# Kernel tuning notes

Hardware: AMD Instinct MI355X
Metric: run time of the kernel (lower is better)

The kernel has to match this reference:

```python
import jax, jax.numpy as jnp
import numpy as np

B, M, D = 16384, 32, 16
LAYERS = [64, 64, 64]


def setup_inputs() -> dict:
    key = jax.random.key(0)
    ks = jax.random.split(key, 4)
    inp = {"embeddings": jax.random.normal(ks[0], (B, M, D), dtype=jnp.float32)}
    hk_1 = M
    for i, hk in enumerate(LAYERS):
        # glorot-ish scale for W_i of shape (m, Hk_1, Hk)
        scale = (2.0 / (M * hk_1 + hk)) ** 0.5
        inp[f"W{i}"] = jax.random.normal(ks[i + 1], (M, hk_1, hk), dtype=jnp.float32) * scale
        hk_1 = hk
    return inp


def reference(embeddings, W0, W1, W2):
    # embeddings == x0: (B, m, D); W_i: (m, Hk_1, Hk)
    x0 = embeddings
    xk = x0  # x^{k-1}, starts as x0 with Hk_1 = m
    outs = []
    for W in (W0, W1, W2):
        # Fused form of: (x0[:,:,None,:] * xk[:,None,:,:])[..., None] * W -> sum over m, Hk_1
        # then permute to (B, Hk, D) and apply activation.
        xk = jax.nn.relu(jnp.einsum("bmd,bhd,mhk->bkd", x0, xk, W))  # (B, Hk, D)
        outs.append(jnp.sum(xk, axis=2))  # (B, Hk)
    return jnp.concatenate(outs, axis=1)  # (B, sum(layers_dim))
```

## Files before the change

### kernel.cpp

```cpp
#include <hip/hip_runtime.h>


typedef _Float16 half8 __attribute__((ext_vector_type(8)));
typedef float f32x4 __attribute__((ext_vector_type(4)));

#define OUT_STRIDE 192

__global__ void prep_w(const float* __restrict__ W, _Float16* __restrict__ dst,
                       int K, int logH, int nkbLog) {
  int e = blockIdx.x * 256 + threadIdx.x;
  int j = e & 7;
  int lane = (e >> 3) & 63;
  int rr = lane & 15, qq = lane >> 4;
  int rest = e >> 9;
  int nkb = K >> 5;
  int kb = rest & (nkb - 1);
  int t = rest >> nkbLog;
  int k = kb * 32 + qq * 8 + j;
  int H = 1 << logH;
  int m = k >> logH, h = k & (H - 1);
  int n = t * 16 + rr;
  dst[e] = (_Float16)W[(m * H + h) * 64 + n];
}

template<int LOGH, int VROW, int VBSTR, bool LAST>
__device__ __forceinline__ void run_layer(
    const _Float16* __restrict__ Wp, const _Float16* vsrc,
    const _Float16* x0s, _Float16* xkdst, float* __restrict__ out,
    long gb0, int loff, int lane, int r, int q)
{
  const int NKB = 1 << LOGH;
  f32x4 acc[4][4];
#pragma unroll
  for (int b = 0; b < 4; ++b)
#pragma unroll
    for (int t = 0; t < 4; ++t) acc[b][t] = (f32x4){0.f, 0.f, 0.f, 0.f};

#pragma unroll 2
  for (int kb = 0; kb < NKB; ++kb) {
    const int m  = kb >> (LOGH - 5);
    const int h0 = (kb & ((1 << (LOGH - 5)) - 1)) << 5;
    half8 Bf[4];
#pragma unroll
    for (int t = 0; t < 4; ++t)
      Bf[t] = *(const half8*)(Wp + ((size_t)(t * NKB + kb) * 64 + lane) * 8);
#pragma unroll
    for (int b = 0; b < 4; ++b) {
      half8 av = *(const half8*)(vsrc + b * VBSTR + r * VROW + h0 + q * 8);
      _Float16 xs = x0s[b * 640 + r * 40 + m];
      half8 xv;
#pragma unroll
      for (int j = 0; j < 8; ++j) xv[j] = xs;
      half8 af = av * xv;
#pragma unroll
      for (int t = 0; t < 4; ++t)
        acc[b][t] = __builtin_amdgcn_mfma_f32_16x16x32_f16(af, Bf[t], acc[b][t], 0, 0, 0);
    }
  }

#pragma unroll
  for (int b = 0; b < 4; ++b) {
#pragma unroll
    for (int t = 0; t < 4; ++t) {
      float s = 0.f;
#pragma unroll
      for (int rr = 0; rr < 4; ++rr) {
        float v = acc[b][t][rr];
        v = v > 0.f ? v : 0.f;
        s += v;
        if (!LAST)
          xkdst[b * 1152 + (q * 4 + rr) * 72 + t * 16 + r] = (_Float16)v;
      }
      s += __shfl_xor(s, 16);
      s += __shfl_xor(s, 32);
      if (q == 0)
        out[(gb0 + b) * OUT_STRIDE + loff + t * 16 + r] = s;
    }
  }
}

__global__ __launch_bounds__(256, 2) void cin_main(
    const float* __restrict__ emb, const _Float16* __restrict__ Wall,
    float* __restrict__ out)
{
  __shared__ __align__(16) _Float16 lds[28672];
  const int lane = threadIdx.x & 63;
  const int wv = threadIdx.x >> 6;
  const int r = lane & 15, q = lane >> 4;
  const int lb0 = wv * 4;
  const long gb0 = (long)blockIdx.x * 16 + lb0;

  _Float16* x0b = &lds[lb0 * 640];
  _Float16* xkb = &lds[10240 + lb0 * 1152];

#pragma unroll
  for (int bb = 0; bb < 4; ++bb) {
    const float* src = emb + (gb0 + bb) * 512;
    _Float16* dstb = x0b + bb * 640;
#pragma unroll
    for (int i = 0; i < 2; ++i) {
      int f = i * 256 + lane * 4;
      float4 v = *(const float4*)(src + f);
      int m = f >> 4, d = f & 15;
      dstb[(d + 0) * 40 + m] = (_Float16)v.x;
      dstb[(d + 1) * 40 + m] = (_Float16)v.y;
      dstb[(d + 2) * 40 + m] = (_Float16)v.z;
      dstb[(d + 3) * 40 + m] = (_Float16)v.w;
    }
  }

  run_layer<5, 40,  640, false>(Wall,           x0b, x0b, xkb, out, gb0, 0,   lane, r, q);
  run_layer<6, 72, 1152, false>(Wall + 65536,   xkb, x0b, xkb, out, gb0, 64,  lane, r, q);
  run_layer<6, 72, 1152, true >(Wall + 196608,  xkb, x0b, xkb, out, gb0, 128, lane, r, q);
}

extern "C" void kernel_launch(void* const* d_in, const int* in_sizes, int n_in,
                              void* d_out, int out_size, void* d_ws, size_t ws_size,
                              hipStream_t stream) {
  const float* emb = (const float*)d_in[0];
  const float* W0  = (const float*)d_in[1];
  const float* W1  = (const float*)d_in[2];
  const float* W2  = (const float*)d_in[3];
  float* out = (float*)d_out;
  _Float16* ws = (_Float16*)d_ws;

  prep_w<<<256, 256, 0, stream>>>(W0, ws,          1024, 5, 5);
  prep_w<<<512, 256, 0, stream>>>(W1, ws + 65536,  2048, 6, 6);
  prep_w<<<512, 256, 0, stream>>>(W2, ws + 196608, 2048, 6, 6);

  cin_main<<<1024, 256, 0, stream>>>(emb, ws, out);
}
```

Baseline: 215.4 us.

## Switch to 32x32x16 MFMA with software-prefetched operands and fused weight prep

Replaces the 16x16x32 MFMA tiling with 32x32x16 MFMAs, so each wave covers two batch rows per instruction and the weight fragment layout is rebuilt to match. Next-iteration weight, activation and x0 operands are loaded one step ahead to hide load latency. The scale multiply now uses packed half2 operations, and LDS strides are padded to reduce bank conflicts. The three weight-prep launches are merged into one kernel to cut launch overhead, at the cost of more accumulator registers per thread and a more complex epilogue index mapping.

```diff
diff --git a/kernel.cpp b/kernel.cpp
--- a/kernel.cpp
+++ b/kernel.cpp
@@ -2,79 +2,143 @@
 
 
 typedef _Float16 half8 __attribute__((ext_vector_type(8)));
-typedef float f32x4 __attribute__((ext_vector_type(4)));
+typedef _Float16 half2v __attribute__((ext_vector_type(2)));
+typedef float f32x16 __attribute__((ext_vector_type(16)));
 
 #define OUT_STRIDE 192
+#define X0B 648
+#define X0R 40
+#define XKB 1160
+#define XKR 72
 
-__global__ void prep_w(const float* __restrict__ W, _Float16* __restrict__ dst,
-                       int K, int logH, int nkbLog) {
+__global__ void prep_w_all(const float* __restrict__ W0,
+                           const float* __restrict__ W1,
+                           const float* __restrict__ W2,
+                           _Float16* __restrict__ dst) {
   int e = blockIdx.x * 256 + threadIdx.x;
-  int j = e & 7;
-  int lane = (e >> 3) & 63;
-  int rr = lane & 15, qq = lane >> 4;
-  int rest = e >> 9;
-  int nkb = K >> 5;
-  int kb = rest & (nkb - 1);
-  int t = rest >> nkbLog;
-  int k = kb * 32 + qq * 8 + j;
-  int H = 1 << logH;
-  int m = k >> logH, h = k & (H - 1);
-  int n = t * 16 + rr;
+  const float* W;
+  int logH, nkbLog, le;
+  if (e < 65536)       { W = W0; logH = 5; nkbLog = 6; le = e; }
+  else if (e < 196608) { W = W1; logH = 6; nkbLog = 7; le = e - 65536; }
+  else                 { W = W2; logH = 6; nkbLog = 7; le = e - 196608; }
+  int j    = le & 7;
+  int lane = (le >> 3) & 63;
+  int rest = le >> 9;
+  int kb   = rest & ((1 << nkbLog) - 1);
+  int t    = rest >> nkbLog;
+  int k    = kb * 16 + ((lane >> 5) << 3) + j;
+  int H    = 1 << logH;
+  int m    = k >> logH, h = k & (H - 1);
+  int n    = t * 32 + (lane & 31);
   dst[e] = (_Float16)W[(m * H + h) * 64 + n];
 }
 
-template<int LOGH, int VROW, int VBSTR, bool LAST>
+template<int LOGH, int VR, int VB, bool LAST>
 __device__ __forceinline__ void run_layer(
     const _Float16* __restrict__ Wp, const _Float16* vsrc,
     const _Float16* x0s, _Float16* xkdst, float* __restrict__ out,
-    long gb0, int loff, int lane, int r, int q)
+    long gb0, int loff, int lane)
 {
-  const int NKB = 1 << LOGH;
-  f32x4 acc[4][4];
+  const int NIT = 1 << (LOGH + 1);
+  const int HM  = (1 << (LOGH - 4)) - 1;
+  const int SH  = LOGH - 4;
+
+  const int l31 = lane & 31;
+  const int q2  = lane >> 5;
+  const int r16 = lane & 15;
+  const int b4  = (lane >> 4) & 1;
+
+  const _Float16* avb[2];
+  const _Float16* xsb[2];
 #pragma unroll
-  for (int b = 0; b < 4; ++b)
+  for (int bp = 0; bp < 2; ++bp) {
+    int bl = bp * 2 + b4;
+    avb[bp] = vsrc + bl * VB + r16 * VR + q2 * 8;
+    xsb[bp] = x0s + bl * X0B + r16 * X0R;
+  }
+  const _Float16* Wl = Wp + lane * 8;
+
+  f32x16 acc[2][2];
 #pragma unroll
-    for (int t = 0; t < 4; ++t) acc[b][t] = (f32x4){0.f, 0.f, 0.f, 0.f};
+  for (int bp = 0; bp < 2; ++bp)
+#pragma unroll
+    for (int t = 0; t < 2; ++t)
+#pragma unroll
+      for (int g = 0; g < 16; ++g) acc[bp][t][g] = 0.f;
 
-#pragma unroll 2
-  for (int kb = 0; kb < NKB; ++kb) {
-    const int m  = kb >> (LOGH - 5);
-    const int h0 = (kb & ((1 << (LOGH - 5)) - 1)) << 5;
-    half8 Bf[4];
+  half8  Bc[2], avc[2];
+  half2v xc[2];
 #pragma unroll
-    for (int t = 0; t < 4; ++t)
-      Bf[t] = *(const half8*)(Wp + ((size_t)(t * NKB + kb) * 64 + lane) * 8);
+  for (int t = 0; t < 2; ++t)
+    Bc[t] = *(const half8*)(Wl + (size_t)(t * NIT) * 512);
 #pragma unroll
-    for (int b = 0; b < 4; ++b) {
-      half8 av = *(const half8*)(vsrc + b * VBSTR + r * VROW + h0 + q * 8);
-      _Float16 xs = x0s[b * 640 + r * 40 + m];
-      half8 xv;
+  for (int bp = 0; bp < 2; ++bp) {
+    avc[bp] = *(const half8*)(avb[bp]);
+    _Float16 x = xsb[bp][0];
+    xc[bp] = (half2v){x, x};
+  }
+
+#pragma unroll 4
+  for (int kb = 0; kb < NIT; ++kb) {
+    half8  Bn[2], avn[2];
+    half2v xn[2];
+    const bool more = (kb + 1) < NIT;
+    if (more) {
+      const int kn = kb + 1;
 #pragma unroll
-      for (int j = 0; j < 8; ++j) xv[j] = xs;
-      half8 af = av * xv;
+      for (int t = 0; t < 2; ++t)
+        Bn[t] = *(const half8*)(Wl + (size_t)(t * NIT + kn) * 512);
+      const int hb = (kn & HM) * 16;
+      const int mn = kn >> SH;
 #pragma unroll
-      for (int t = 0; t < 4; ++t)
-        acc[b][t] = __builtin_amdgcn_mfma_f32_16x16x32_f16(af, Bf[t], acc[b][t], 0, 0, 0);
+      for (int bp = 0; bp < 2; ++bp) {
+        avn[bp] = *(const half8*)(avb[bp] + hb);
+        _Float16 x = xsb[bp][mn];
+        xn[bp] = (half2v){x, x};
+      }
+    }
+    half8 af[2];
+#pragma unroll
+    for (int bp = 0; bp < 2; ++bp) {
+      half2v* ap = (half2v*)&af[bp];
+      half2v* vp = (half2v*)&avc[bp];
+#pragma unroll
+      for (int j2 = 0; j2 < 4; ++j2) ap[j2] = vp[j2] * xc[bp];
+    }
+#pragma unroll
+    for (int bp = 0; bp < 2; ++bp)
+#pragma unroll
+      for (int t = 0; t < 2; ++t)
+        acc[bp][t] = __builtin_amdgcn_mfma_f32_32x32x16_f16(
+            af[bp], Bc[t], acc[bp][t], 0, 0, 0);
+    if (more) {
+#pragma unroll
+      for (int t = 0; t < 2; ++t) Bc[t] = Bn[t];
+#pragma unroll
+      for (int bp = 0; bp < 2; ++bp) { avc[bp] = avn[bp]; xc[bp] = xn[bp]; }
     }
   }
 
 #pragma unroll
-  for (int b = 0; b < 4; ++b) {
+  for (int bp = 0; bp < 2; ++bp) {
 #pragma unroll
-    for (int t = 0; t < 4; ++t) {
-      float s = 0.f;
+    for (int t = 0; t < 2; ++t) {
+      float s[2] = {0.f, 0.f};
 #pragma unroll
-      for (int rr = 0; rr < 4; ++rr) {
-        float v = acc[b][t][rr];
+      for (int g = 0; g < 16; ++g) {
+        float v = acc[bp][t][g];
         v = v > 0.f ? v : 0.f;
-        s += v;
+        const int half = g >> 3;
+        const int g7 = g & 7;
+        const int d = (g7 & 3) + 8 * (g7 >> 2) + 4 * q2;
+        s[half] += v;
         if (!LAST)
-          xkdst[b * 1152 + (q * 4 + rr) * 72 + t * 16 + r] = (_Float16)v;
+          xkdst[(bp * 2 + half) * XKB + d * XKR + t * 32 + l31] = (_Float16)v;
       }
-      s += __shfl_xor(s, 16);
-      s += __shfl_xor(s, 32);
-      if (q == 0)
-        out[(gb0 + b) * OUT_STRIDE + loff + t * 16 + r] = s;
+      s[0] += __shfl_xor(s[0], 32);
+      s[1] += __shfl_xor(s[1], 32);
+      const float sv = q2 ? s[1] : s[0];
+      out[(gb0 + bp * 2 + q2) * OUT_STRIDE + loff + t * 32 + l31] = sv;
     }
   }
 }
@@ -83,35 +147,33 @@
     const float* __restrict__ emb, const _Float16* __restrict__ Wall,
     float* __restrict__ out)
 {
-  __shared__ __align__(16) _Float16 lds[28672];
+  __shared__ __align__(16) _Float16 lds[16 * X0B + 16 * XKB];
   const int lane = threadIdx.x & 63;
   const int wv = threadIdx.x >> 6;
-  const int r = lane & 15, q = lane >> 4;
-  const int lb0 = wv * 4;
-  const long gb0 = (long)blockIdx.x * 16 + lb0;
+  const long gb0 = (long)blockIdx.x * 16 + wv * 4;
 
-  _Float16* x0b = &lds[lb0 * 640];
-  _Float16* xkb = &lds[10240 + lb0 * 1152];
+  _Float16* x0w = &lds[wv * 4 * X0B];
+  _Float16* xkw = &lds[16 * X0B + wv * 4 * XKB];
 
 #pragma unroll
   for (int bb = 0; bb < 4; ++bb) {
     const float* src = emb + (gb0 + bb) * 512;
-    _Float16* dstb = x0b + bb * 640;
+    _Float16* dstb = x0w + bb * X0B;
 #pragma unroll
     for (int i = 0; i < 2; ++i) {
       int f = i * 256 + lane * 4;
       float4 v = *(const float4*)(src + f);
       int m = f >> 4, d = f & 15;
-      dstb[(d + 0) * 40 + m] = (_Float16)v.x;
-      dstb[(d + 1) * 40 + m] = (_Float16)v.y;
-      dstb[(d + 2) * 40 + m] = (_Float16)v.z;
-      dstb[(d + 3) * 40 + m] = (_Float16)v.w;
+      dstb[(d + 0) * X0R + m] = (_Float16)v.x;
+      dstb[(d + 1) * X0R + m] = (_Float16)v.y;
+      dstb[(d + 2) * X0R + m] = (_Float16)v.z;
+      dstb[(d + 3) * X0R + m] = (_Float16)v.w;
     }
   }
 
-  run_layer<5, 40,  640, false>(Wall,           x0b, x0b, xkb, out, gb0, 0,   lane, r, q);
-  run_layer<6, 72, 1152, false>(Wall + 65536,   xkb, x0b, xkb, out, gb0, 64,  lane, r, q);
-  run_layer<6, 72, 1152, true >(Wall + 196608,  xkb, x0b, xkb, out, gb0, 128, lane, r, q);
+  run_layer<5, X0R, X0B, false>(Wall,          x0w, x0w, xkw, out, gb0, 0,   lane);
+  run_layer<6, XKR, XKB, false>(Wall + 65536,  xkw, x0w, xkw, out, gb0, 64,  lane);
+  run_layer<6, XKR, XKB, true >(Wall + 196608, xkw, x0w, xkw, out, gb0, 128, lane);
 }
 
 extern "C" void kernel_launch(void* const* d_in, const int* in_sizes, int n_in,
@@ -124,9 +186,7 @@
   float* out = (float*)d_out;
   _Float16* ws = (_Float16*)d_ws;
 
-  prep_w<<<256, 256, 0, stream>>>(W0, ws,          1024, 5, 5);
-  prep_w<<<512, 256, 0, stream>>>(W1, ws + 65536,  2048, 6, 6);
-  prep_w<<<512, 256, 0, stream>>>(W2, ws + 196608, 2048, 6, 6);
+  prep_w_all<<<1280, 256, 0, stream>>>(W0, W1, W2, ws);
 
   cin_main<<<1024, 256, 0, stream>>>(emb, ws, out);
 }
```

Result: slower. 241.1 us (+11.9%).

## Hoist xk fragments into registers, fuse weight prep launches, raise occupancy

Applied to the files above, without the earlier changes.

The A-operand vectors (x0 and xk rows) are now loaded from LDS into registers once per layer rather than every k-block, and the m loop is restructured so the x0 scalar broadcast is loaded once per m and multiplied with packed half2 ops. The three weight-prep kernels are merged into one launch, and the x0 LDS row stride shrinks from 40 to 32 with launch bounds raised to 3 blocks per CU. The aim is to cut LDS traffic, launch overhead and latency exposure, at the cost of more register pressure and possible LDS bank conflicts from the unpadded stride.

```diff
diff --git a/kernel.cpp b/kernel.cpp
--- a/kernel.cpp
+++ b/kernel.cpp
@@ -2,59 +2,80 @@
 
 
 typedef _Float16 half8 __attribute__((ext_vector_type(8)));
+typedef _Float16 half2v __attribute__((ext_vector_type(2)));
 typedef float f32x4 __attribute__((ext_vector_type(4)));
 
 #define OUT_STRIDE 192
+#define X0R 32
+#define X0B 512
+#define XKR 72
+#define XKB 1152
 
-__global__ void prep_w(const float* __restrict__ W, _Float16* __restrict__ dst,
-                       int K, int logH, int nkbLog) {
+__global__ void prep_w_all(const float* __restrict__ W0,
+                           const float* __restrict__ W1,
+                           const float* __restrict__ W2,
+                           _Float16* __restrict__ dst) {
   int e = blockIdx.x * 256 + threadIdx.x;
-  int j = e & 7;
-  int lane = (e >> 3) & 63;
-  int rr = lane & 15, qq = lane >> 4;
-  int rest = e >> 9;
-  int nkb = K >> 5;
-  int kb = rest & (nkb - 1);
-  int t = rest >> nkbLog;
-  int k = kb * 32 + qq * 8 + j;
-  int H = 1 << logH;
-  int m = k >> logH, h = k & (H - 1);
-  int n = t * 16 + rr;
+  const float* W;
+  int logH, nkbLog, le;
+  if (e < 65536)       { W = W0; logH = 5; nkbLog = 5; le = e; }
+  else if (e < 196608) { W = W1; logH = 6; nkbLog = 6; le = e - 65536; }
+  else                 { W = W2; logH = 6; nkbLog = 6; le = e - 196608; }
+  int j    = le & 7;
+  int lane = (le >> 3) & 63;
+  int rr   = lane & 15, qq = lane >> 4;
+  int rest = le >> 9;
+  int kb   = rest & ((1 << nkbLog) - 1);
+  int t    = rest >> nkbLog;
+  int k    = kb * 32 + qq * 8 + j;
+  int H    = 1 << logH;
+  int m    = k >> logH, h = k & (H - 1);
+  int n    = t * 16 + rr;
   dst[e] = (_Float16)W[(m * H + h) * 64 + n];
 }
 
-template<int LOGH, int VROW, int VBSTR, bool LAST>
+template<int NHI, bool LAST>
 __device__ __forceinline__ void run_layer(
-    const _Float16* __restrict__ Wp, const _Float16* vsrc,
-    const _Float16* x0s, _Float16* xkdst, float* __restrict__ out,
+    const _Float16* __restrict__ Wp, const half8 (&av)[4][NHI],
+    const _Float16* x0s, _Float16* xkw, float* __restrict__ out,
     long gb0, int loff, int lane, int r, int q)
 {
-  const int NKB = 1 << LOGH;
+  const int NKB = 32 * NHI;
   f32x4 acc[4][4];
 #pragma unroll
   for (int b = 0; b < 4; ++b)
 #pragma unroll
     for (int t = 0; t < 4; ++t) acc[b][t] = (f32x4){0.f, 0.f, 0.f, 0.f};
 
+  const _Float16* Wl = Wp + lane * 8;
+
 #pragma unroll 2
-  for (int kb = 0; kb < NKB; ++kb) {
-    const int m  = kb >> (LOGH - 5);
-    const int h0 = (kb & ((1 << (LOGH - 5)) - 1)) << 5;
-    half8 Bf[4];
-#pragma unroll
-    for (int t = 0; t < 4; ++t)
-      Bf[t] = *(const half8*)(Wp + ((size_t)(t * NKB + kb) * 64 + lane) * 8);
+  for (int m = 0; m < 32; ++m) {
+    half2v xs2[4];
 #pragma unroll
     for (int b = 0; b < 4; ++b) {
-      half8 av = *(const half8*)(vsrc + b * VBSTR + r * VROW + h0 + q * 8);
-      _Float16 xs = x0s[b * 640 + r * 40 + m];
-      half8 xv;
+      _Float16 x = x0s[b * X0B + r * X0R + m];
+      xs2[b] = (half2v){x, x};
+    }
 #pragma unroll
-      for (int j = 0; j < 8; ++j) xv[j] = xs;
-      half8 af = av * xv;
+    for (int hi = 0; hi < NHI; ++hi) {
+      const int kb = m * NHI + hi;
+      half8 Bf[4];
 #pragma unroll
       for (int t = 0; t < 4; ++t)
-        acc[b][t] = __builtin_amdgcn_mfma_f32_16x16x32_f16(af, Bf[t], acc[b][t], 0, 0, 0);
+        Bf[t] = *(const half8*)(Wl + (size_t)(t * NKB + kb) * 512);
+#pragma unroll
+      for (int b = 0; b < 4; ++b) {
+        half8 af;
+        half2v* ap = (half2v*)&af;
+        const half2v* vp = (const half2v*)&av[b][hi];
+#pragma unroll
+        for (int j2 = 0; j2 < 4; ++j2) ap[j2] = vp[j2] * xs2[b];
+#pragma unroll
+        for (int t = 0; t < 4; ++t)
+          acc[b][t] = __builtin_amdgcn_mfma_f32_16x16x32_f16(
+              af, Bf[t], acc[b][t], 0, 0, 0);
+      }
     }
   }
 
@@ -69,7 +90,7 @@
         v = v > 0.f ? v : 0.f;
         s += v;
         if (!LAST)
-          xkdst[b * 1152 + (q * 4 + rr) * 72 + t * 16 + r] = (_Float16)v;
+          xkw[b * XKB + (q * 4 + rr) * XKR + t * 16 + r] = (_Float16)v;
       }
       s += __shfl_xor(s, 16);
       s += __shfl_xor(s, 32);
@@ -79,39 +100,55 @@
   }
 }
 
-__global__ __launch_bounds__(256, 2) void cin_main(
+__global__ __launch_bounds__(256, 3) void cin_main(
     const float* __restrict__ emb, const _Float16* __restrict__ Wall,
     float* __restrict__ out)
 {
-  __shared__ __align__(16) _Float16 lds[28672];
+  __shared__ __align__(16) _Float16 lds[16 * X0B + 16 * XKB];
   const int lane = threadIdx.x & 63;
   const int wv = threadIdx.x >> 6;
   const int r = lane & 15, q = lane >> 4;
-  const int lb0 = wv * 4;
-  const long gb0 = (long)blockIdx.x * 16 + lb0;
+  const long gb0 = (long)blockIdx.x * 16 + wv * 4;
 
-  _Float16* x0b = &lds[lb0 * 640];
-  _Float16* xkb = &lds[10240 + lb0 * 1152];
+  _Float16* x0w = &lds[wv * 4 * X0B];
+  _Float16* xkw = &lds[16 * X0B + wv * 4 * XKB];
 
 #pragma unroll
   for (int bb = 0; bb < 4; ++bb) {
     const float* src = emb + (gb0 + bb) * 512;
-    _Float16* dstb = x0b + bb * 640;
+    _Float16* dstb = x0w + bb * X0B;
 #pragma unroll
     for (int i = 0; i < 2; ++i) {
       int f = i * 256 + lane * 4;
       float4 v = *(const float4*)(src + f);
       int m = f >> 4, d = f & 15;
-      dstb[(d + 0) * 40 + m] = (_Float16)v.x;
-      dstb[(d + 1) * 40 + m] = (_Float16)v.y;
-      dstb[(d + 2) * 40 + m] = (_Float16)v.z;
-      dstb[(d + 3) * 40 + m] = (_Float16)v.w;
+      dstb[(d + 0) * X0R + m] = (_Float16)v.x;
+      dstb[(d + 1) * X0R + m] = (_Float16)v.y;
+      dstb[(d + 2) * X0R + m] = (_Float16)v.z;
+      dstb[(d + 3) * X0R + m] = (_Float16)v.w;
     }
   }
 
-  run_layer<5, 40,  640, false>(Wall,           x0b, x0b, xkb, out, gb0, 0,   lane, r, q);
-  run_layer<6, 72, 1152, false>(Wall + 65536,   xkb, x0b, xkb, out, gb0, 64,  lane, r, q);
-  run_layer<6, 72, 1152, true >(Wall + 196608,  xkb, x0b, xkb, out, gb0, 128, lane, r, q);
+  half8 av1[4][1];
+#pragma unroll
+  for (int b = 0; b < 4; ++b)
+    av1[b][0] = *(const half8*)(x0w + b * X0B + r * X0R + q * 8);
+  run_layer<1, false>(Wall, av1, x0w, xkw, out, gb0, 0, lane, r, q);
+
+  half8 av2[4][2];
+#pragma unroll
+  for (int b = 0; b < 4; ++b)
+#pragma unroll
+    for (int hi = 0; hi < 2; ++hi)
+      av2[b][hi] = *(const half8*)(xkw + b * XKB + r * XKR + hi * 32 + q * 8);
+  run_layer<2, false>(Wall + 65536, av2, x0w, xkw, out, gb0, 64, lane, r, q);
+
+#pragma unroll
+  for (int b = 0; b < 4; ++b)
+#pragma unroll
+    for (int hi = 0; hi < 2; ++hi)
+      av2[b][hi] = *(const half8*)(xkw + b * XKB + r * XKR + hi * 32 + q * 8);
+  run_layer<2, true>(Wall + 196608, av2, x0w, xkw, out, gb0, 128, lane, r, q);
 }
 
 extern "C" void kernel_launch(void* const* d_in, const int* in_sizes, int n_in,
@@ -124,9 +161,7 @@
   float* out = (float*)d_out;
   _Float16* ws = (_Float16*)d_ws;
 
-  prep_w<<<256, 256, 0, stream>>>(W0, ws,          1024, 5, 5);
-  prep_w<<<512, 256, 0, stream>>>(W1, ws + 65536,  2048, 6, 6);
-  prep_w<<<512, 256, 0, stream>>>(W2, ws + 196608, 2048, 6, 6);
+  prep_w_all<<<1280, 256, 0, stream>>>(W0, W1, W2, ws);
 
   cin_main<<<1024, 256, 0, stream>>>(emb, ws, out);
 }
```

Result: faster. 206.4 us (-4.2%).
